# Kernel optimization log

Hardware: AMD Instinct MI355X
Metric: run time of the kernel (lower is better)

## Reference

```python
import jax, jax.numpy as jnp
import numpy as np

N_NODES = 100000
N_EDGES = 1600000
IN_FEAT = 64
OUT_FEAT = 64
K_ORDER = 1
BN_EPS = 1e-5


def setup_inputs() -> dict:
    key = jax.random.key(0)
    ks = jax.random.split(key, 8)
    feature = jax.random.normal(ks[0], (N_NODES, IN_FEAT), dtype=jnp.float32)
    sp_embeddings = jax.random.normal(ks[1], (N_NODES, 16), dtype=jnp.float32)
    edge_src = jax.random.randint(ks[2], (N_EDGES,), 0, N_NODES, dtype=jnp.int32)
    edge_dst = jax.random.randint(ks[3], (N_EDGES,), 0, N_NODES, dtype=jnp.int32)
    edge_order = jax.random.randint(ks[4], (N_EDGES,), 0, K_ORDER + 1, dtype=jnp.int32)
    # xavier_normal over (in, out) fan dims
    std = float(np.sqrt(2.0 / (IN_FEAT + OUT_FEAT)))
    linear = jax.random.normal(ks[5], (K_ORDER + 1, IN_FEAT, OUT_FEAT), dtype=jnp.float32) * std
    mlp_w = jax.random.normal(ks[6], (OUT_FEAT, OUT_FEAT), dtype=jnp.float32) * std
    mlp_b = jnp.zeros((OUT_FEAT,), dtype=jnp.float32)
    bn_gamma = jnp.ones((OUT_FEAT,), dtype=jnp.float32)
    bn_beta = jnp.zeros((OUT_FEAT,), dtype=jnp.float32)
    return {
        "feature": feature,
        "sp_embeddings": sp_embeddings,
        "linear": linear,
        "mlp_w": mlp_w,
        "mlp_b": mlp_b,
        "bn_gamma": bn_gamma,
        "bn_beta": bn_beta,
        "edge_src": edge_src,
        "edge_dst": edge_dst,
        "edge_order": edge_order,
    }


def reference(feature, sp_embeddings, linear, mlp_w, mlp_b, bn_gamma, bn_beta,
              edge_src, edge_dst, edge_order):
    # msg_fun: gather per-edge weight matrix by edge order, batched matvec
    W_e = linear[edge_order]          # [E, in, out]
    h_src = feature[edge_src]          # [E, in]
    msg = jnp.einsum('eio,ei->eo', W_e, h_src)  # [E, out]
    # agg_fun: scatter-sum messages into destination nodes
    h = jax.ops.segment_sum(msg, edge_dst, num_segments=N_NODES)  # [N, out]
    # mlp: Linear -> ReLU -> BatchNorm1d (training mode: batch stats)
    h = jax.nn.relu(h @ mlp_w.T + mlp_b)
    mean = jnp.mean(h, axis=0)
    var = jnp.var(h, axis=0)  # biased, matching torch BN normalization
    h = (h - mean) * jax.lax.rsqrt(var + BN_EPS) * bn_gamma + bn_beta
    # shortcut=False -> no residual; sp_embeddings unused by forward
    return h
```

## Files before the change

kernel.cpp:

```cpp
#include <hip/hip_runtime.h>

#define N_NODES 100000
#define N_EDGES 1600000
#define NBUCK 1563
#define NBLK 128
#define PER_BLK 12500
#define MAX_BE 2048


__device__ __forceinline__ unsigned short f2bf(float x) {
  unsigned u = __float_as_uint(x);
  unsigned r = (u + 0x7FFFu + ((u >> 16) & 1u)) >> 16;
  return (unsigned short)r;
}

__global__ __launch_bounds__(256) void prep_U(const float* __restrict__ linear,
                                              const float* __restrict__ mlp_w,
                                              float* __restrict__ U) {
  int idx = blockIdx.x * 256 + threadIdx.x;
  int o = idx & 63;
  int ki = idx >> 6;
  int k = ki >> 6, i = ki & 63;
  float acc = 0.f;
#pragma unroll 8
  for (int j = 0; j < 64; ++j)
    acc += linear[ki * 64 + j] * mlp_w[o * 64 + j];
  U[i * 128 + k * 64 + o] = acc;
}

__global__ __launch_bounds__(256) void prep_B(const float* __restrict__ feature,
                                              const float* __restrict__ U,
                                              unsigned short* __restrict__ B) {
  __shared__ float Us[64 * 128];
  for (int i = threadIdx.x; i < 64 * 128; i += 256) Us[i] = U[i];
  __syncthreads();
  int row = blockIdx.x * 256 + threadIdx.x;
  if (row >= N_NODES) return;
  const float4* Fr = reinterpret_cast<const float4*>(feature + (size_t)row * 64);
#pragma unroll
  for (int k = 0; k < 2; ++k) {
    float acc[64];
#pragma unroll
    for (int o = 0; o < 64; ++o) acc[o] = 0.f;
#pragma unroll 4
    for (int i4 = 0; i4 < 16; ++i4) {
      float4 a = Fr[i4];
      float av[4] = {a.x, a.y, a.z, a.w};
#pragma unroll
      for (int u = 0; u < 4; ++u) {
        const float* Ur = &Us[(i4 * 4 + u) * 128 + k * 64];
#pragma unroll
        for (int o = 0; o < 64; ++o) acc[o] = fmaf(av[u], Ur[o], acc[o]);
      }
    }
    ushort4* Bp = reinterpret_cast<ushort4*>(B + (((size_t)row * 2 + k) << 6));
#pragma unroll
    for (int o4 = 0; o4 < 16; ++o4) {
      ushort4 pk;
      pk.x = f2bf(acc[o4 * 4 + 0]);
      pk.y = f2bf(acc[o4 * 4 + 1]);
      pk.z = f2bf(acc[o4 * 4 + 2]);
      pk.w = f2bf(acc[o4 * 4 + 3]);
      Bp[o4] = pk;
    }
  }
}

__global__ __launch_bounds__(256) void countA(const int* __restrict__ edst,
                                              unsigned* __restrict__ cntg) {
  __shared__ unsigned h[NBUCK];
  for (int i = threadIdx.x; i < NBUCK; i += 256) h[i] = 0;
  __syncthreads();
  const int k = blockIdx.x;
  const int beg = k * PER_BLK, end = beg + PER_BLK;
  for (int e = beg + (int)threadIdx.x; e < end; e += 256)
    atomicAdd(&h[((unsigned)edst[e]) >> 6], 1u);
  __syncthreads();
  for (int i = threadIdx.x; i < NBUCK; i += 256)
    cntg[(size_t)k * NBUCK + i] = h[i];
}

__global__ __launch_bounds__(256) void scanT1(unsigned* __restrict__ cntg,
                                              unsigned* __restrict__ tot) {
  const int lane = threadIdx.x & 63;
  const int wv = threadIdx.x >> 6;
  const int b = blockIdx.x * 4 + wv;
  if (b >= NBUCK) return;
  unsigned c0 = cntg[(size_t)lane * NBUCK + b];
  unsigned c1 = cntg[(size_t)(64 + lane) * NBUCK + b];
  unsigned i0 = c0, i1 = c1;
#pragma unroll
  for (int d = 1; d < 64; d <<= 1) {
    unsigned n0 = __shfl_up(i0, d);
    unsigned n1 = __shfl_up(i1, d);
    if (lane >= d) { i0 += n0; i1 += n1; }
  }
  unsigned tot0 = __shfl(i0, 63);
  unsigned tot1 = __shfl(i1, 63);
  cntg[(size_t)lane * NBUCK + b] = i0 - c0;
  cntg[(size_t)(64 + lane) * NBUCK + b] = tot0 + i1 - c1;
  if (lane == 0) tot[b] = tot0 + tot1;
}

__global__ __launch_bounds__(256) void scanT2(const unsigned* __restrict__ tot,
                                              unsigned* __restrict__ base) {
  __shared__ unsigned sh[256];
  const int t = threadIdx.x;
  unsigned local[7];
  unsigned s = 0;
#pragma unroll
  for (int i = 0; i < 7; ++i) {
    int idx = t * 7 + i;
    local[i] = (idx < NBUCK) ? tot[idx] : 0u;
    s += local[i];
  }
  sh[t] = s;
  __syncthreads();
#pragma unroll
  for (int off = 1; off < 256; off <<= 1) {
    unsigned v = (t >= off) ? sh[t - off] : 0u;
    __syncthreads();
    sh[t] += v;
    __syncthreads();
  }
  unsigned run = sh[t] - s;
#pragma unroll
  for (int i = 0; i < 7; ++i) {
    int idx = t * 7 + i;
    if (idx < NBUCK) { base[idx] = run; run += local[i]; }
  }
  if (t == 0) base[NBUCK] = N_EDGES;
}

__global__ __launch_bounds__(256) void fillB(const int* __restrict__ esrc,
                                             const int* __restrict__ edst,
                                             const int* __restrict__ eord,
                                             const unsigned* __restrict__ cntg,
                                             const unsigned* __restrict__ base,
                                             unsigned* __restrict__ pay) {
  __shared__ unsigned curL[NBUCK];
  const int k = blockIdx.x;
  for (int i = threadIdx.x; i < NBUCK; i += 256)
    curL[i] = base[i] + cntg[(size_t)k * NBUCK + i];
  __syncthreads();
  const int beg = k * PER_BLK, end = beg + PER_BLK;
  for (int e = beg + (int)threadIdx.x; e < end; e += 256) {
    unsigned d = (unsigned)edst[e];
    unsigned pos = atomicAdd(&curL[d >> 6], 1u);
    pay[pos] = ((d & 63u) << 18) | ((unsigned)esrc[e] << 1) | (unsigned)eord[e];
  }
}

__global__ __launch_bounds__(256) void bgather(const unsigned* __restrict__ base,
                                               const unsigned* __restrict__ pay,
                                               const unsigned short* __restrict__ B,
                                               const float* __restrict__ bias,
                                               float* __restrict__ out,
                                               double* __restrict__ stats) {
  __shared__ unsigned hist[64];
  __shared__ unsigned offsL[65];
  __shared__ unsigned curN[64];
  __shared__ unsigned pay_s[MAX_BE];
  __shared__ double dred[4][64];
  const int lane = threadIdx.x & 63;
  const int wv = threadIdx.x >> 6;
  const int b = blockIdx.x;
  const unsigned base0 = base[b];
  const unsigned n_e = base[b + 1] - base0;

  if (threadIdx.x < 64) hist[threadIdx.x] = 0;
  __syncthreads();
  for (unsigned i = threadIdx.x; i < n_e; i += 256)
    atomicAdd(&hist[pay[base0 + i] >> 18], 1u);
  __syncthreads();
  if (wv == 0) {
    unsigned hv = hist[lane];
    unsigned inc = hv;
#pragma unroll
    for (int d = 1; d < 64; d <<= 1) {
      unsigned n = __shfl_up(inc, d);
      if (lane >= d) inc += n;
    }
    offsL[lane + 1] = inc;
    if (lane == 0) offsL[0] = 0;
    curN[lane] = inc - hv;
  }
  __syncthreads();
  for (unsigned i = threadIdx.x; i < n_e; i += 256) {
    unsigned w = pay[base0 + i];
    unsigned pos = atomicAdd(&curN[w >> 18], 1u);
    pay_s[pos] = w;
  }
  __syncthreads();

  const float bo = bias[lane];
  double s0 = 0.0, s1 = 0.0;
  const int nb0 = (b << 6) + wv * 16;

  if (nb0 < N_NODES) {
    unsigned offv = (lane <= 16) ? offsL[wv * 16 + lane] : 0u;
    unsigned e = (unsigned)__shfl((int)offv, 0);
    const unsigned eEnd = (unsigned)__shfl((int)offv, 16);
    int c = 0;
    unsigned next_end = (unsigned)__shfl((int)offv, 1);
    float sum = 0.f;

#define FLUSH()                                                         \
    do {                                                                \
      float val = fmaxf(sum + bo, 0.f);                                 \
      out[((size_t)(nb0 + c) << 6) + lane] = val;                       \
      s0 += (double)val;                                                \
      s1 += (double)val * (double)val;                                  \
      sum = 0.f;                                                        \
      ++c;                                                              \
      next_end = (unsigned)__shfl((int)offv, min(c + 1, 16));           \
    } while (0)

    while (e < eEnd) {
      unsigned rem = eEnd - e;
      int cnt = rem < 16u ? (int)rem : 16;
      unsigned p[16];
      unsigned short v[16];
#pragma unroll
      for (int j = 0; j < 16; ++j)
        p[j] = pay_s[e + (j < cnt ? j : 0)];
#pragma unroll
      for (int j = 0; j < 16; ++j)
        v[j] = B[((size_t)(p[j] & 0x3FFFFu) << 6) + lane];
#pragma unroll
      for (int j = 0; j < 16; ++j) {
        if (j < cnt) {
          while (e + (unsigned)j == next_end) FLUSH();
          sum += __uint_as_float((unsigned)v[j] << 16);
        }
      }
      e += cnt;
    }
    for (; c < 16; ++c) {
      float val = fmaxf(sum + bo, 0.f);
      out[((size_t)(nb0 + c) << 6) + lane] = val;
      s0 += (double)val;
      s1 += (double)val * (double)val;
      sum = 0.f;
    }
#undef FLUSH
  }

  dred[wv][lane] = s0;
  __syncthreads();
  if (wv == 0) {
    double t = dred[0][lane] + dred[1][lane] + dred[2][lane] + dred[3][lane];
    atomicAdd(&stats[lane], t);
  }
  __syncthreads();
  dred[wv][lane] = s1;
  __syncthreads();
  if (wv == 0) {
    double t = dred[0][lane] + dred[1][lane] + dred[2][lane] + dred[3][lane];
    atomicAdd(&stats[64 + lane], t);
  }
}

__global__ __launch_bounds__(256) void bn_apply(float* __restrict__ h,
                                                const double* __restrict__ stats,
                                                const float* __restrict__ gamma,
                                                const float* __restrict__ beta) {
  const int lane = threadIdx.x & 63;
  double mean = stats[lane] * (1.0 / N_NODES);
  double var = stats[64 + lane] * (1.0 / N_NODES) - mean * mean;
  float inv = (float)(1.0 / sqrt(var + 1e-5));
  float scale = gamma[lane] * inv;
  float shift = beta[lane] - (float)mean * scale;
  int wid = (blockIdx.x * 256 + threadIdx.x) >> 6;
  const int nw = gridDim.x * 4;
  for (int r = wid; r < N_NODES; r += nw) {
    size_t idx = ((size_t)r << 6) + lane;
    h[idx] = h[idx] * scale + shift;
  }
}

extern "C" void kernel_launch(void* const* d_in, const int* in_sizes, int n_in,
                              void* d_out, int out_size, void* d_ws, size_t ws_size,
                              hipStream_t stream) {
  const float* feature = (const float*)d_in[0];
  const float* linear = (const float*)d_in[2];
  const float* mlp_w  = (const float*)d_in[3];
  const float* mlp_b  = (const float*)d_in[4];
  const float* gamma  = (const float*)d_in[5];
  const float* beta   = (const float*)d_in[6];
  const int* esrc = (const int*)d_in[7];
  const int* edst = (const int*)d_in[8];
  const int* eord = (const int*)d_in[9];
  float* out = (float*)d_out;

  char* basep = (char*)d_ws;
  unsigned*       cntg  = (unsigned*)(basep);
  unsigned*       tot   = (unsigned*)(basep + 800256);
  unsigned*       base  = (unsigned*)(basep + 806512);
  double*         stats = (double*)  (basep + 812800);
  float*          U     = (float*)   (basep + 813824);
  unsigned*       pay   = (unsigned*)(basep + 846592);
  unsigned short* B     = (unsigned short*)(basep + 7246592);

  hipMemsetAsync(stats, 0, 1024, stream);
  prep_U<<<32, 256, 0, stream>>>(linear, mlp_w, U);
  countA<<<NBLK, 256, 0, stream>>>(edst, cntg);
  scanT1<<<(NBUCK + 3) / 4, 256, 0, stream>>>(cntg, tot);
  scanT2<<<1, 256, 0, stream>>>(tot, base);
  fillB<<<NBLK, 256, 0, stream>>>(esrc, edst, eord, cntg, base, pay);
  prep_B<<<(N_NODES + 255) / 256, 256, 0, stream>>>(feature, U, B);
  bgather<<<NBUCK, 256, 0, stream>>>(base, pay, B, mlp_b, out, stats);
  bn_apply<<<1024, 256, 0, stream>>>(out, stats, gamma, beta);
}
```

Measured before the change: 186.4 us.

## Remap gather to 16-lane groups with 8-byte bf16 loads per node

The bucketed gather kernel now assigns each 16-thread group four nodes, and each thread gathers four bf16 columns at once with a uint2 load. Previously a whole wavefront walked 16 nodes serially, one column per lane. The change also replaces the per-edge flush/shuffle logic with simple per-node loops, writes float4 outputs, and reduces the BN statistics with xor-shuffles plus one shared-memory pass. It aims for wider memory transactions and more independent rows in flight. The cost is that load balance now varies with per-node degree inside each 16-lane group, so lanes in a wave can diverge.

```diff
diff --git a/kernel.cpp b/kernel.cpp
--- a/kernel.cpp
+++ b/kernel.cpp
@@ -161,16 +161,18 @@
   __shared__ unsigned offsL[65];
   __shared__ unsigned curN[64];
   __shared__ unsigned pay_s[MAX_BE];
-  __shared__ double dred[4][64];
-  const int lane = threadIdx.x & 63;
-  const int wv = threadIdx.x >> 6;
+  __shared__ double dd0[4][64];
+  __shared__ double dd1[4][64];
+  const int tid = threadIdx.x;
+  const int lane = tid & 63;
+  const int wv = tid >> 6;
   const int b = blockIdx.x;
   const unsigned base0 = base[b];
   const unsigned n_e = base[b + 1] - base0;
 
-  if (threadIdx.x < 64) hist[threadIdx.x] = 0;
-  __syncthreads();
-  for (unsigned i = threadIdx.x; i < n_e; i += 256)
+  if (tid < 64) hist[tid] = 0;
+  __syncthreads();
+  for (unsigned i = tid; i < n_e; i += 256)
     atomicAdd(&hist[pay[base0 + i] >> 18], 1u);
   __syncthreads();
   if (wv == 0) {
@@ -186,78 +188,83 @@
     curN[lane] = inc - hv;
   }
   __syncthreads();
-  for (unsigned i = threadIdx.x; i < n_e; i += 256) {
+  for (unsigned i = tid; i < n_e; i += 256) {
     unsigned w = pay[base0 + i];
     unsigned pos = atomicAdd(&curN[w >> 18], 1u);
     pay_s[pos] = w;
   }
   __syncthreads();
 
-  const float bo = bias[lane];
-  double s0 = 0.0, s1 = 0.0;
-  const int nb0 = (b << 6) + wv * 16;
-
-  if (nb0 < N_NODES) {
-    unsigned offv = (lane <= 16) ? offsL[wv * 16 + lane] : 0u;
-    unsigned e = (unsigned)__shfl((int)offv, 0);
-    const unsigned eEnd = (unsigned)__shfl((int)offv, 16);
-    int c = 0;
-    unsigned next_end = (unsigned)__shfl((int)offv, 1);
-    float sum = 0.f;
-
-#define FLUSH()                                                         \
-    do {                                                                \
-      float val = fmaxf(sum + bo, 0.f);                                 \
-      out[((size_t)(nb0 + c) << 6) + lane] = val;                       \
-      s0 += (double)val;                                                \
-      s1 += (double)val * (double)val;                                  \
-      sum = 0.f;                                                        \
-      ++c;                                                              \
-      next_end = (unsigned)__shfl((int)offv, min(c + 1, 16));           \
-    } while (0)
-
-    while (e < eEnd) {
-      unsigned rem = eEnd - e;
-      int cnt = rem < 16u ? (int)rem : 16;
-      unsigned p[16];
-      unsigned short v[16];
-#pragma unroll
-      for (int j = 0; j < 16; ++j)
-        p[j] = pay_s[e + (j < cnt ? j : 0)];
-#pragma unroll
-      for (int j = 0; j < 16; ++j)
-        v[j] = B[((size_t)(p[j] & 0x3FFFFu) << 6) + lane];
-#pragma unroll
-      for (int j = 0; j < 16; ++j) {
+  const int g = tid >> 4;
+  const int sl = tid & 15;
+  const int c0 = sl << 2;
+  const float4 bo4 = *reinterpret_cast<const float4*>(bias + c0);
+  double s0[4] = {0, 0, 0, 0}, s1[4] = {0, 0, 0, 0};
+
+#pragma unroll
+  for (int i = 0; i < 4; ++i) {
+    const int nl = (g << 2) + i;
+    const int ng = (b << 6) + nl;
+    unsigned e = offsL[nl];
+    const unsigned e1 = offsL[nl + 1];
+    float s[4] = {0.f, 0.f, 0.f, 0.f};
+    while (e < e1) {
+      unsigned rem = e1 - e;
+      int cnt = rem < 8u ? (int)rem : 8;
+      unsigned p[8];
+      uint2 v[8];
+#pragma unroll
+      for (int j = 0; j < 8; ++j)
+        p[j] = pay_s[e + (j < cnt ? (unsigned)j : 0u)];
+#pragma unroll
+      for (int j = 0; j < 8; ++j)
+        v[j] = *reinterpret_cast<const uint2*>(
+            B + (((size_t)(p[j] & 0x3FFFFu)) << 6) + c0);
+#pragma unroll
+      for (int j = 0; j < 8; ++j) {
         if (j < cnt) {
-          while (e + (unsigned)j == next_end) FLUSH();
-          sum += __uint_as_float((unsigned)v[j] << 16);
+          s[0] += __uint_as_float(v[j].x << 16);
+          s[1] += __uint_as_float(v[j].x & 0xFFFF0000u);
+          s[2] += __uint_as_float(v[j].y << 16);
+          s[3] += __uint_as_float(v[j].y & 0xFFFF0000u);
         }
       }
       e += cnt;
     }
-    for (; c < 16; ++c) {
-      float val = fmaxf(sum + bo, 0.f);
-      out[((size_t)(nb0 + c) << 6) + lane] = val;
-      s0 += (double)val;
-      s1 += (double)val * (double)val;
-      sum = 0.f;
-    }
-#undef FLUSH
-  }
-
-  dred[wv][lane] = s0;
-  __syncthreads();
-  if (wv == 0) {
-    double t = dred[0][lane] + dred[1][lane] + dred[2][lane] + dred[3][lane];
-    atomicAdd(&stats[lane], t);
-  }
-  __syncthreads();
-  dred[wv][lane] = s1;
-  __syncthreads();
-  if (wv == 0) {
-    double t = dred[0][lane] + dred[1][lane] + dred[2][lane] + dred[3][lane];
-    atomicAdd(&stats[64 + lane], t);
+    if (ng < N_NODES) {
+      float4 r;
+      r.x = fmaxf(s[0] + bo4.x, 0.f);
+      r.y = fmaxf(s[1] + bo4.y, 0.f);
+      r.z = fmaxf(s[2] + bo4.z, 0.f);
+      r.w = fmaxf(s[3] + bo4.w, 0.f);
+      *reinterpret_cast<float4*>(out + ((size_t)ng << 6) + c0) = r;
+      s0[0] += (double)r.x; s1[0] += (double)r.x * (double)r.x;
+      s0[1] += (double)r.y; s1[1] += (double)r.y * (double)r.y;
+      s0[2] += (double)r.z; s1[2] += (double)r.z * (double)r.z;
+      s0[3] += (double)r.w; s1[3] += (double)r.w * (double)r.w;
+    }
+  }
+
+#pragma unroll
+  for (int q = 0; q < 4; ++q) {
+    double v0 = s0[q], v1 = s1[q];
+    v0 += __shfl_xor(v0, 16); v0 += __shfl_xor(v0, 32);
+    v1 += __shfl_xor(v1, 16); v1 += __shfl_xor(v1, 32);
+    s0[q] = v0; s1[q] = v1;
+  }
+  if ((lane & 48) == 0) {
+#pragma unroll
+    for (int q = 0; q < 4; ++q) {
+      dd0[wv][c0 + q] = s0[q];
+      dd1[wv][c0 + q] = s1[q];
+    }
+  }
+  __syncthreads();
+  if (tid < 64) {
+    double t0 = dd0[0][tid] + dd0[1][tid] + dd0[2][tid] + dd0[3][tid];
+    double t1 = dd1[0][tid] + dd1[1][tid] + dd1[2][tid] + dd1[3][tid];
+    atomicAdd(&stats[tid], t0);
+    atomicAdd(&stats[64 + tid], t1);
   }
 }
 
```

New measurement: 178.9 us. -4.0%, faster.
